# Kernel tuning notes

Measured on AMD Instinct MI355X. Metric: run time of the kernel, lower is better.

Reference implementation:

```python
import jax, jax.numpy as jnp
import numpy as np


def _bilinear_resample(imgs, dvfs):
    # imgs: (B,H,W,C), dvfs: (B,H,W,2) with channel 0 = x(width) offset, 1 = y(height) offset
    B, H, W, C = imgs.shape
    fx = jnp.arange(W, dtype=imgs.dtype)[None, None, :] + dvfs[..., 0]  # (B,H,W)
    fy = jnp.arange(H, dtype=imgs.dtype)[None, :, None] + dvfs[..., 1]  # (B,H,W)

    x0f = jnp.floor(fx)
    y0f = jnp.floor(fy)
    wx = fx - x0f  # fractional weights
    wy = fy - y0f
    x0 = x0f.astype(jnp.int32)
    y0 = y0f.astype(jnp.int32)
    x1 = x0 + 1
    y1 = y0 + 1

    def gather(iy, ix):
        # zero-padding semantics for out-of-bounds corners (tf resampler behavior)
        valid = (ix >= 0) & (ix < W) & (iy >= 0) & (iy < H)
        ixc = jnp.clip(ix, 0, W - 1)
        iyc = jnp.clip(iy, 0, H - 1)
        vals = jax.vmap(lambda im, yy, xx: im[yy, xx])(imgs, iyc, ixc)  # (B,H,W,C)
        return vals * valid[..., None].astype(imgs.dtype)

    v00 = gather(y0, x0)
    v01 = gather(y0, x1)
    v10 = gather(y1, x0)
    v11 = gather(y1, x1)

    wx = wx[..., None]
    wy = wy[..., None]
    return (v00 * (1 - wx) * (1 - wy)
            + v01 * wx * (1 - wy)
            + v10 * (1 - wx) * wy
            + v11 * wx * wy)


def setup_inputs() -> dict:
    key = jax.random.key(0)
    k1, k2 = jax.random.split(key)
    B, H, W = 32, 1024, 1024
    imgs = jax.random.normal(k1, (B, H, W, 1), dtype=jnp.float32)
    dvfs = jax.random.normal(k2, (B, H, W, 2), dtype=jnp.float32)
    return {"imgs": imgs, "dvfs": dvfs}


def reference(imgs, dvfs):
    return _bilinear_resample(imgs, dvfs)
```

## Files before the change

kernel.cpp:

```cpp
#include <hip/hip_runtime.h>
#include <hip/hip_bf16.h>


#define H_DIM 1024
#define W_DIM 1024

__device__ __forceinline__ float gather_zp(const float* __restrict__ img,
                                           int yy, int xx) {
    bool valid = (xx >= 0) & (xx < W_DIM) & (yy >= 0) & (yy < H_DIM);
    int xc = min(max(xx, 0), W_DIM - 1);
    int yc = min(max(yy, 0), H_DIM - 1);
    float v = img[yc * W_DIM + xc];
    return valid ? v : 0.0f;
}

__global__ __launch_bounds__(256) void bilerp_kernel(
        const float* __restrict__ imgs,
        const float* __restrict__ dvfs,
        float* __restrict__ out,
        long long total_pixels) {
    long long tid = (long long)blockIdx.x * blockDim.x + threadIdx.x;
    long long base = tid * 4;
    if (base >= total_pixels) return;

    const int hw = H_DIM * W_DIM;
    int b   = (int)(base / hw);
    int rem = (int)(base % hw);
    int y   = rem / W_DIM;
    int x   = rem % W_DIM;

    const float* __restrict__ img = imgs + (long long)b * hw;

    const float4* dvf4 = (const float4*)(dvfs + base * 2);
    float4 d0 = dvf4[0];
    float4 d1 = dvf4[1];
    float dx[4] = {d0.x, d0.z, d1.x, d1.z};
    float dy[4] = {d0.y, d0.w, d1.y, d1.w};

    float4 res;
    float* rp = &res.x;
    #pragma unroll
    for (int i = 0; i < 4; ++i) {
        float fx = (float)(x + i) + dx[i];
        float fy = (float)y       + dy[i];
        float x0f = floorf(fx);
        float y0f = floorf(fy);
        float wx = fx - x0f;
        float wy = fy - y0f;
        int x0 = (int)x0f;
        int y0 = (int)y0f;
        int x1 = x0 + 1;
        int y1 = y0 + 1;

        float v00 = gather_zp(img, y0, x0);
        float v01 = gather_zp(img, y0, x1);
        float v10 = gather_zp(img, y1, x0);
        float v11 = gather_zp(img, y1, x1);

        rp[i] = v00 * (1.0f - wx) * (1.0f - wy)
              + v01 * wx          * (1.0f - wy)
              + v10 * (1.0f - wx) * wy
              + v11 * wx          * wy;
    }

    *(float4*)(out + base) = res;
}

extern "C" void kernel_launch(void* const* d_in, const int* in_sizes, int n_in,
                              void* d_out, int out_size, void* d_ws, size_t ws_size,
                              hipStream_t stream) {
    const float* imgs = (const float*)d_in[0];
    const float* dvfs = (const float*)d_in[1];
    float* out = (float*)d_out;

    long long total_pixels = (long long)out_size;
    long long n_threads = (total_pixels + 3) / 4;
    int block = 256;
    long long grid = (n_threads + block - 1) / block;

    bilerp_kernel<<<(dim3)(unsigned)grid, block, 0, stream>>>(imgs, dvfs, out, total_pixels);
}
```

Before: 531.6 us.

## Use 2D 128x8 tiles with XCD-aware block swizzle and nontemporal streaming

Each block now covers a 2D tile of 128x8 pixels instead of a linear run of 1024 pixels, so gather footprints from neighboring rows overlap within a block. Block indices are remapped so that consecutive chunks of tiles land on the same XCD, which is meant to improve L2 reuse of the image. The dvfs loads and output stores become nontemporal so streaming data does not evict image lines from cache. This assumes the pixel count is divisible by 8192 and that H and W match the fixed tile sizes.

```diff
diff --git a/kernel.cpp b/kernel.cpp
--- a/kernel.cpp
+++ b/kernel.cpp
@@ -4,6 +4,12 @@
 
 #define H_DIM 1024
 #define W_DIM 1024
+#define TILE_W 128
+#define TILE_H 8
+#define TY_N (H_DIM / TILE_H)
+#define TX_N (W_DIM / TILE_W)
+
+typedef float vf4 __attribute__((ext_vector_type(4)));
 
 __device__ __forceinline__ float gather_zp(const float* __restrict__ img,
                                            int yy, int xx) {
@@ -18,27 +24,30 @@
         const float* __restrict__ imgs,
         const float* __restrict__ dvfs,
         float* __restrict__ out,
-        long long total_pixels) {
-    long long tid = (long long)blockIdx.x * blockDim.x + threadIdx.x;
-    long long base = tid * 4;
-    if (base >= total_pixels) return;
+        int nblocks) {
+    int j = blockIdx.x;
+    int chunk = nblocks >> 3;
+    int v = (j & 7) * chunk + (j >> 3);
 
-    const int hw = H_DIM * W_DIM;
-    int b   = (int)(base / hw);
-    int rem = (int)(base % hw);
-    int y   = rem / W_DIM;
-    int x   = rem % W_DIM;
+    int ty   = v % TY_N;
+    int rest = v / TY_N;
+    int tx   = rest % TX_N;
+    int b    = rest / TX_N;
 
-    const float* __restrict__ img = imgs + (long long)b * hw;
+    int t = threadIdx.x;
+    int x = tx * TILE_W + (t & 31) * 4;
+    int y = ty * TILE_H + (t >> 5);
 
-    const float4* dvf4 = (const float4*)(dvfs + base * 2);
-    float4 d0 = dvf4[0];
-    float4 d1 = dvf4[1];
+    const float* __restrict__ img = imgs + (size_t)b * (H_DIM * W_DIM);
+    size_t pix = ((size_t)b * H_DIM + y) * W_DIM + x;
+
+    const vf4* dvf4 = (const vf4*)(dvfs + pix * 2);
+    vf4 d0 = __builtin_nontemporal_load(dvf4);
+    vf4 d1 = __builtin_nontemporal_load(dvf4 + 1);
     float dx[4] = {d0.x, d0.z, d1.x, d1.z};
     float dy[4] = {d0.y, d0.w, d1.y, d1.w};
 
-    float4 res;
-    float* rp = &res.x;
+    vf4 res;
     #pragma unroll
     for (int i = 0; i < 4; ++i) {
         float fx = (float)(x + i) + dx[i];
@@ -57,13 +66,13 @@
         float v10 = gather_zp(img, y1, x0);
         float v11 = gather_zp(img, y1, x1);
 
-        rp[i] = v00 * (1.0f - wx) * (1.0f - wy)
-              + v01 * wx          * (1.0f - wy)
-              + v10 * (1.0f - wx) * wy
-              + v11 * wx          * wy;
+        res[i] = v00 * (1.0f - wx) * (1.0f - wy)
+               + v01 * wx          * (1.0f - wy)
+               + v10 * (1.0f - wx) * wy
+               + v11 * wx          * wy;
     }
 
-    *(float4*)(out + base) = res;
+    __builtin_nontemporal_store(res, (vf4*)(out + pix));
 }
 
 extern "C" void kernel_launch(void* const* d_in, const int* in_sizes, int n_in,
@@ -73,10 +82,8 @@
     const float* dvfs = (const float*)d_in[1];
     float* out = (float*)d_out;
 
-    long long total_pixels = (long long)out_size;
-    long long n_threads = (total_pixels + 3) / 4;
-    int block = 256;
-    long long grid = (n_threads + block - 1) / block;
+    int px_per_block = 256 * 4;
+    int nblocks = out_size / px_per_block;
 
-    bilerp_kernel<<<(dim3)(unsigned)grid, block, 0, stream>>>(imgs, dvfs, out, total_pixels);
+    bilerp_kernel<<<nblocks, 256, 0, stream>>>(imgs, dvfs, out, nblocks);
 }
```

New measurement: 555.5 us. +4.5%, slower.
